# Performance work log

Hardware: AMD Instinct MI355X
Metric: run time of the kernel (lower is better)

Reference implementation:

```python
import jax, jax.numpy as jnp
import numpy as np

ALIGN_CORNERS = True   # module init arg
NUM_AUX = 8            # auxiliary samples for linearized multi-sampling
NOISE_STRENGTH = 0.5   # noise scale in units of input pixel spacing
EPS = 1e-6             # Tikhonov term for the per-pixel 2x2 least squares


def _base_coords(n, align_corners):
    if align_corners:
        return jnp.linspace(-1.0, 1.0, n, dtype=jnp.float32)
    return (jnp.arange(n, dtype=jnp.float32) * 2.0 + 1.0) / n - 1.0


def affine_grid(theta, h_out, w_out, align_corners):
    # theta: [B,2,3] -> grid [B,h_out,w_out,2] with (x,y) in [-1,1]
    xs = _base_coords(w_out, align_corners)
    ys = _base_coords(h_out, align_corners)
    X, Y = jnp.meshgrid(xs, ys)                      # [H,W]
    base = jnp.stack([X, Y, jnp.ones_like(X)], -1)   # [H,W,3]
    return jnp.einsum('hwk,bik->bhwi', base, theta)  # [B,H,W,2]


def bilinear_sample(image, grid, align_corners):
    # image [B,C,Hi,Wi], grid [B,H,W,2] -> [B,H,W,C], zero padding outside
    B, C, Hi, Wi = image.shape
    x, y = grid[..., 0], grid[..., 1]
    if align_corners:
        ix = (x + 1.0) * 0.5 * (Wi - 1)
        iy = (y + 1.0) * 0.5 * (Hi - 1)
    else:
        ix = ((x + 1.0) * Wi - 1.0) * 0.5
        iy = ((y + 1.0) * Hi - 1.0) * 0.5
    x0 = jnp.floor(ix); y0 = jnp.floor(iy)
    wx1 = ix - x0; wy1 = iy - y0
    bidx = jnp.arange(B)[:, None, None]

    def tap(xi, yi, w):
        valid = (xi >= 0) & (xi <= Wi - 1) & (yi >= 0) & (yi <= Hi - 1)
        xc = jnp.clip(xi, 0, Wi - 1).astype(jnp.int32)
        yc = jnp.clip(yi, 0, Hi - 1).astype(jnp.int32)
        v = image[bidx, :, yc, xc]                   # [B,H,W,C] gather
        return v * (w * valid)[..., None]

    return (tap(x0, y0, (1 - wx1) * (1 - wy1)) +
            tap(x0 + 1, y0, wx1 * (1 - wy1)) +
            tap(x0, y0 + 1, (1 - wx1) * wy1) +
            tap(x0 + 1, y0 + 1, wx1 * wy1))


def linearized_grid_sample(image, grid, align_corners):
    # Linearized multi-sampling (Jiang et al., ICCV'19): forward value equals
    # the center bilinear sample; gradient wrt grid flows through a per-pixel
    # least-squares linearization fitted from NUM_AUX noisy auxiliary samples.
    B, C, Hi, Wi = image.shape
    key = jax.random.key(42)
    spacing = jnp.array([2.0 / Wi, 2.0 / Hi], dtype=jnp.float32)  # one input pixel in norm coords
    g0 = jax.lax.stop_gradient(grid)
    noise = jax.random.normal(key, (B, NUM_AUX) + grid.shape[1:3] + (2,), dtype=jnp.float32)
    aux = g0[:, None] + noise * NOISE_STRENGTH * spacing          # [B,K,H,W,2]

    center = bilinear_sample(image, g0, align_corners)            # [B,H,W,C]
    samp = jax.vmap(lambda g: bilinear_sample(image, g, align_corners),
                    in_axes=1, out_axes=1)(aux)                   # [B,K,H,W,C]

    d_int = samp - center[:, None]                                # [B,K,H,W,C]
    d_grid = aux - g0[:, None]                                    # [B,K,H,W,2]
    xtx = jnp.einsum('bkhwi,bkhwj->bhwij', d_grid, d_grid) \
        + EPS * jnp.eye(2, dtype=jnp.float32)                     # [B,H,W,2,2]
    xty = jnp.einsum('bkhwi,bkhwc->bhwic', d_grid, d_int)         # [B,H,W,2,C]
    slope = jnp.linalg.solve(xtx, xty)                            # [B,H,W,2,C]

    out = center + jnp.einsum('bhwic,bhwi->bhwc', slope, grid - g0)
    return jnp.transpose(out, (0, 3, 1, 2))                       # [B,C,H,W]


def setup_inputs() -> dict:
    key = jax.random.key(0)
    k1, k2 = jax.random.split(key)
    B, C, Hi, Wi = 4, 3, 1024, 1024
    image = jax.random.normal(k1, (B, C, Hi, Wi), dtype=jnp.float32)
    ident = jnp.tile(jnp.array([[1.0, 0.0, 0.0], [0.0, 1.0, 0.0]], dtype=jnp.float32), (B, 1, 1))
    pMtrx = ident + 0.05 * jax.random.normal(k2, (B, 2, 3), dtype=jnp.float32)
    return {"image": image, "pMtrx": pMtrx, "W": 1024, "H": 1024}


def reference(image, pMtrx, W, H):
    # torch.affine_grid_generator(pMtrx, (B,3,W,H)) -> grid [B, W, H, 2]
    grid = affine_grid(pMtrx, W, H, ALIGN_CORNERS)
    return linearized_grid_sample(image, grid, ALIGN_CORNERS)  # [B,C,W,H]
```

## Files before the change

kernel.cpp:

```cpp
#include <hip/hip_runtime.h>


#define B_  4
#define C_  3
#define HI  1024
#define WI  1024
#define HO  1024
#define WO  1024

#define TW  32
#define TH  32
#define MAXSEG  13
#define MAXROWS 48

typedef __attribute__((address_space(3))) void* lds_vp;
typedef const __attribute__((address_space(1))) void* gbl_vp;

__device__ __forceinline__ float2 map_px(int w, int h,
                                         float t0, float t1, float t2,
                                         float t3, float t4, float t5) {
    const float xs = -1.0f + 2.0f * (float)w / (float)(WO - 1);
    const float ys = -1.0f + 2.0f * (float)h / (float)(HO - 1);
    const float x = t0 * xs + (t1 * ys + t2);
    const float y = t3 * xs + (t4 * ys + t5);
    const float ix = (x + 1.0f) * 0.5f * (float)(WI - 1);
    const float iy = (y + 1.0f) * 0.5f * (float)(HI - 1);
    return make_float2(ix, iy);
}

__global__ __launch_bounds__(256) void warp_bilinear_fast_kernel(
    const float* __restrict__ image,
    const float* __restrict__ theta,
    float* __restrict__ out)
{
    __shared__ float lds[7680];

    const int bid = blockIdx.x;
    const int sid = ((bid & 7) << 9) | (bid >> 3);

    const int b   = sid >> 10;
    const int rem = sid & 1023;
    const int h0  = (rem >> 5) * TH;
    const int w0  = (rem & 31) * TW;

    const float* t = theta + b * 6;
    const float t0 = t[0], t1 = t[1], t2 = t[2];
    const float t3 = t[3], t4 = t[4], t5 = t[5];

    const float2 c00 = map_px(w0,        h0,        t0,t1,t2,t3,t4,t5);
    const float2 c10 = map_px(w0+TW-1,   h0,        t0,t1,t2,t3,t4,t5);
    const float2 c01 = map_px(w0,        h0+TH-1,   t0,t1,t2,t3,t4,t5);
    const float2 c11 = map_px(w0+TW-1,   h0+TH-1,   t0,t1,t2,t3,t4,t5);

    const float ixmin = fminf(fminf(c00.x, c10.x), fminf(c01.x, c11.x));
    const float iymin = fminf(fminf(c00.y, c10.y), fminf(c01.y, c11.y));
    const float ixmax = fmaxf(fmaxf(c00.x, c10.x), fmaxf(c01.x, c11.x));
    const float iymax = fmaxf(fmaxf(c00.y, c10.y), fmaxf(c01.y, c11.y));

    int xlo = (int)floorf(ixmin) - 1;
    int xhi = (int)floorf(ixmax) + 2;
    xlo = min(max(xlo, 0), WI - 1);
    xhi = min(max(xhi, xlo), WI - 1);
    int bx = xlo & ~3;
    const int nseg = min((xhi - bx + 4) >> 2, MAXSEG);
    bx = min(bx, WI - 4 * nseg);

    int ylo = (int)floorf(iymin) - 1;
    int yhi = (int)floorf(iymax) + 2;
    ylo = min(max(ylo, 0), HI - 1);
    yhi = min(max(yhi, ylo), HI - 1);
    const int nrows = min(yhi - ylo + 1, MAXROWS);
    const int by = min(ylo, HI - nrows);

    const int rowf   = nseg << 2;
    const int segch  = nrows * nseg;
    const int segtot = C_ * segch;
    const int chf    = segch << 2;

    const float rcp_segch = 1.0f / (float)segch;
    const float rcp_nseg  = 1.0f / (float)nseg;

    const float* imgb = image + (size_t)b * (C_ * HI * WI);

    const int wv   = threadIdx.x >> 6;
    const int lane = threadIdx.x & 63;
    const int niter = (segtot + 63) >> 6;
    for (int j = wv; j < niter; j += 4) {
        const int seg = (j << 6) + lane;
        if (seg < segtot) {
            const int c  = (int)(((float)seg + 0.5f) * rcp_segch);
            const int r2 = seg - c * segch;
            const int r  = (int)(((float)r2 + 0.5f) * rcp_nseg);
            const int s  = r2 - r * nseg;
            const float* gp = imgb + c * (HI * WI) + (by + r) * WI + (bx + (s << 2));
            __builtin_amdgcn_global_load_lds((gbl_vp)gp, (lds_vp)(lds + (j << 8)),
                                             16, 0, 0);
        }
    }
    __syncthreads();

    const int wloc = threadIdx.x & 31;
    const int tyq  = threadIdx.x >> 5;
    const int w    = w0 + wloc;

    float* ob = out + (size_t)b * (C_ * HO * WO) + w;

    const bool interior = (ixmin >= 1.0f) && (ixmax <= (float)(WI - 2)) &&
                          (iymin >= 1.0f) && (iymax <= (float)(HI - 2));

    if (interior) {
#pragma unroll
        for (int k = 0; k < 4; ++k) {
            const int h = h0 + tyq + 8 * k;
            const float2 ixy = map_px(w, h, t0, t1, t2, t3, t4, t5);
            const float ix = ixy.x, iy = ixy.y;

            const float x0f = floorf(ix);
            const float y0f = floorf(iy);
            const float wx1 = ix - x0f;
            const float wy1 = iy - y0f;
            const float wx0 = 1.0f - wx1;
            const float wy0 = 1.0f - wy1;

            const float w00 = wx0 * wy0, w10 = wx1 * wy0;
            const float w01 = wx0 * wy1, w11 = wx1 * wy1;

            const int ox = (int)x0f - bx;
            const int oy = (int)y0f - by;
            const float* base0 = lds + oy * rowf + ox;

#pragma unroll
            for (int c = 0; c < C_; ++c) {
                const float* p = base0 + c * chf;
                const float v = p[0]        * w00 + p[1]        * w10
                              + p[rowf]     * w01 + p[rowf + 1] * w11;
                __builtin_nontemporal_store(v, ob + c * (HO * WO) + h * WO);
            }
        }
    } else {
#pragma unroll
        for (int k = 0; k < 4; ++k) {
            const int h = h0 + tyq + 8 * k;
            const float2 ixy = map_px(w, h, t0, t1, t2, t3, t4, t5);
            const float ix = ixy.x, iy = ixy.y;

            const float x0f = floorf(ix);
            const float y0f = floorf(iy);
            const float wx1 = ix - x0f;
            const float wy1 = iy - y0f;
            const int x0 = (int)x0f;
            const int y0 = (int)y0f;

            const float ax0 = (1.0f - wx1) * ((x0 >= 0 && x0 <= WI - 1) ? 1.0f : 0.0f);
            const float ax1 = wx1          * ((x0 >= -1 && x0 <= WI - 2) ? 1.0f : 0.0f);
            const float ay0 = (1.0f - wy1) * ((y0 >= 0 && y0 <= HI - 1) ? 1.0f : 0.0f);
            const float ay1 = wy1          * ((y0 >= -1 && y0 <= HI - 2) ? 1.0f : 0.0f);

            const float w00 = ax0 * ay0, w10 = ax1 * ay0;
            const float w01 = ax0 * ay1, w11 = ax1 * ay1;

            const int bw = (nseg << 2) - 1;
            const int xl0 = min(max(min(max(x0,     0), WI - 1) - bx, 0), bw);
            const int xl1 = min(max(min(max(x0 + 1, 0), WI - 1) - bx, 0), bw);
            const int yl0 = min(max(min(max(y0,     0), HI - 1) - by, 0), nrows - 1);
            const int yl1 = min(max(min(max(y0 + 1, 0), HI - 1) - by, 0), nrows - 1);

            const int o00 = yl0 * rowf + xl0;
            const int o10 = yl0 * rowf + xl1;
            const int o01 = yl1 * rowf + xl0;
            const int o11 = yl1 * rowf + xl1;

#pragma unroll
            for (int c = 0; c < C_; ++c) {
                const float* p = lds + c * chf;
                const float v = p[o00] * w00 + p[o10] * w10
                              + p[o01] * w01 + p[o11] * w11;
                __builtin_nontemporal_store(v, ob + c * (HO * WO) + h * WO);
            }
        }
    }
}

extern "C" void kernel_launch(void* const* d_in, const int* in_sizes, int n_in,
                              void* d_out, int out_size, void* d_ws, size_t ws_size,
                              hipStream_t stream) {
    const float* image = (const float*)d_in[0];
    const float* theta = (const float*)d_in[1];
    float* out = (float*)d_out;

    const int grid = B_ * (HO / TH) * (WO / TW);
    warp_bilinear_fast_kernel<<<grid, 256, 0, stream>>>(image, theta, out);
}
```

Before: 110.4 us.

## Reshape tiles to 64x16 and emit 4-wide vectorized nontemporal output stores

```diff
diff --git a/kernel.cpp b/kernel.cpp
--- a/kernel.cpp
+++ b/kernel.cpp
@@ -8,13 +8,14 @@
 #define HO  1024
 #define WO  1024
 
-#define TW  32
-#define TH  32
-#define MAXSEG  13
-#define MAXROWS 48
+#define TW  64
+#define TH  16
+#define MAXSEG  21
+#define MAXROWS 32
 
 typedef __attribute__((address_space(3))) void* lds_vp;
 typedef const __attribute__((address_space(1))) void* gbl_vp;
+typedef float f32x4 __attribute__((ext_vector_type(4)));
 
 __device__ __forceinline__ float2 map_px(int w, int h,
                                          float t0, float t1, float t2,
@@ -33,15 +34,15 @@
     const float* __restrict__ theta,
     float* __restrict__ out)
 {
-    __shared__ float lds[7680];
+    __shared__ float lds[MAXSEG * 4 * MAXROWS * C_];
 
     const int bid = blockIdx.x;
     const int sid = ((bid & 7) << 9) | (bid >> 3);
 
     const int b   = sid >> 10;
     const int rem = sid & 1023;
-    const int h0  = (rem >> 5) * TH;
-    const int w0  = (rem & 31) * TW;
+    const int h0  = (rem >> 4) * TH;
+    const int w0  = (rem & 15) * TW;
 
     const float* t = theta + b * 6;
     const float t0 = t[0], t1 = t[1], t2 = t[2];
@@ -99,21 +100,31 @@
     }
     __syncthreads();
 
-    const int wloc = threadIdx.x & 31;
-    const int tyq  = threadIdx.x >> 5;
-    const int w    = w0 + wloc;
-
-    float* ob = out + (size_t)b * (C_ * HO * WO) + w;
+    const int qx  = threadIdx.x & 15;
+    const int row = threadIdx.x >> 4;
+    const int h   = h0 + row;
+    const int wq  = w0 + (qx << 2);
+
+    const float ys = -1.0f + 2.0f * (float)h / (float)(HO - 1);
+    const float xb = t1 * ys + t2;
+    const float yb = t4 * ys + t5;
+
+    float* ob = out + (size_t)b * (C_ * HO * WO) + h * WO + wq;
+
+    float o0[4], o1[4], o2[4];
 
     const bool interior = (ixmin >= 1.0f) && (ixmax <= (float)(WI - 2)) &&
                           (iymin >= 1.0f) && (iymax <= (float)(HI - 2));
 
     if (interior) {
 #pragma unroll
-        for (int k = 0; k < 4; ++k) {
-            const int h = h0 + tyq + 8 * k;
-            const float2 ixy = map_px(w, h, t0, t1, t2, t3, t4, t5);
-            const float ix = ixy.x, iy = ixy.y;
+        for (int px = 0; px < 4; ++px) {
+            const int w = wq + px;
+            const float xs = -1.0f + 2.0f * (float)w / (float)(WO - 1);
+            const float x = t0 * xs + xb;
+            const float y = t3 * xs + yb;
+            const float ix = (x + 1.0f) * 0.5f * (float)(WI - 1);
+            const float iy = (y + 1.0f) * 0.5f * (float)(HI - 1);
 
             const float x0f = floorf(ix);
             const float y0f = floorf(iy);
@@ -129,20 +140,31 @@
             const int oy = (int)y0f - by;
             const float* base0 = lds + oy * rowf + ox;
 
-#pragma unroll
-            for (int c = 0; c < C_; ++c) {
-                const float* p = base0 + c * chf;
-                const float v = p[0]        * w00 + p[1]        * w10
-                              + p[rowf]     * w01 + p[rowf + 1] * w11;
-                __builtin_nontemporal_store(v, ob + c * (HO * WO) + h * WO);
+            {
+                const float* p = base0;
+                o0[px] = p[0]    * w00 + p[1]        * w10
+                       + p[rowf] * w01 + p[rowf + 1] * w11;
+            }
+            {
+                const float* p = base0 + chf;
+                o1[px] = p[0]    * w00 + p[1]        * w10
+                       + p[rowf] * w01 + p[rowf + 1] * w11;
+            }
+            {
+                const float* p = base0 + 2 * chf;
+                o2[px] = p[0]    * w00 + p[1]        * w10
+                       + p[rowf] * w01 + p[rowf + 1] * w11;
             }
         }
     } else {
 #pragma unroll
-        for (int k = 0; k < 4; ++k) {
-            const int h = h0 + tyq + 8 * k;
-            const float2 ixy = map_px(w, h, t0, t1, t2, t3, t4, t5);
-            const float ix = ixy.x, iy = ixy.y;
+        for (int px = 0; px < 4; ++px) {
+            const int w = wq + px;
+            const float xs = -1.0f + 2.0f * (float)w / (float)(WO - 1);
+            const float x = t0 * xs + xb;
+            const float y = t3 * xs + yb;
+            const float ix = (x + 1.0f) * 0.5f * (float)(WI - 1);
+            const float iy = (y + 1.0f) * 0.5f * (float)(HI - 1);
 
             const float x0f = floorf(ix);
             const float y0f = floorf(iy);
@@ -170,15 +192,21 @@
             const int o01 = yl1 * rowf + xl0;
             const int o11 = yl1 * rowf + xl1;
 
-#pragma unroll
-            for (int c = 0; c < C_; ++c) {
-                const float* p = lds + c * chf;
-                const float v = p[o00] * w00 + p[o10] * w10
-                              + p[o01] * w01 + p[o11] * w11;
-                __builtin_nontemporal_store(v, ob + c * (HO * WO) + h * WO);
-            }
+            o0[px] = lds[o00] * w00 + lds[o10] * w10
+                   + lds[o01] * w01 + lds[o11] * w11;
+            o1[px] = lds[chf + o00] * w00 + lds[chf + o10] * w10
+                   + lds[chf + o01] * w01 + lds[chf + o11] * w11;
+            o2[px] = lds[2*chf + o00] * w00 + lds[2*chf + o10] * w10
+                   + lds[2*chf + o01] * w01 + lds[2*chf + o11] * w11;
         }
     }
+
+    f32x4 s0 = { o0[0], o0[1], o0[2], o0[3] };
+    f32x4 s1 = { o1[0], o1[1], o1[2], o1[3] };
+    f32x4 s2 = { o2[0], o2[1], o2[2], o2[3] };
+    __builtin_nontemporal_store(s0, (f32x4*)(ob));
+    __builtin_nontemporal_store(s1, (f32x4*)(ob + (size_t)(HO * WO)));
+    __builtin_nontemporal_store(s2, (f32x4*)(ob + (size_t)(2 * HO * WO)));
 }
 
 extern "C" void kernel_launch(void* const* d_in, const int* in_sizes, int n_in,
```

New measurement: 109.0 us. Within noise of the previous version (-1.2%).
